# Optimization experiments

Measured on AMD Instinct MI355X. Metric: run time of the kernel, lower is better.

The kernel has to match this reference:

```python
import jax, jax.numpy as jnp
import numpy as np

B, C, N = 128, 256, 4096
CQ = C // 4
BN_EPS = 1e-5


def setup_inputs() -> dict:
    key = jax.random.key(0)
    ks = jax.random.split(key, 12)
    w = lambda k, shape: jax.random.normal(k, shape, dtype=jnp.float32) * 0.05
    return {
        "x": jax.random.normal(ks[0], (B, C, N), dtype=jnp.float32),
        "x_key": jax.random.normal(ks[1], (B, C, 1), dtype=jnp.float32),
        "wq": w(ks[2], (CQ, C)), "bq": jnp.zeros((CQ,), jnp.float32),
        "wk": w(ks[3], (CQ, C)), "bk": jnp.zeros((CQ,), jnp.float32),
        "wv": w(ks[4], (C, C)),  "bv": jnp.zeros((C,), jnp.float32),
        "wt": w(ks[5], (C, C)),  "bt": jnp.zeros((C,), jnp.float32),
        "gamma": jnp.ones((C,), jnp.float32),
        "beta": jnp.zeros((C,), jnp.float32),
    }


def reference(x, x_key, wq, bq, wk, bk, wv, bv, wt, bt, gamma, beta):
    # 1x1 convs are per-point linear maps over the channel dim.
    x_q = jnp.einsum('oc,bcn->bno', wq, x) + bq              # (B, N, C/4)
    x_k = jnp.einsum('oc,bcn->bo', wk, x_key) + bk           # (B, C/4)  (length-1 key)
    x_v = jnp.einsum('oc,bcn->bon', wv, x) + bv[None, :, None]  # (B, C, N)

    # tanh-gated QK: energy over the N points against the single key.
    energy = jnp.einsum('bno,bo->bn', jnp.tanh(x_q), jnp.tanh(x_k))  # (B, N)
    attention = jax.nn.softmax(energy, axis=-1)                       # (B, N)

    # context: attention-weighted sum of V -> single point per batch.
    x_r = jnp.einsum('bcn,bn->bc', x_v, attention)[..., None]  # (B, C, 1)

    # trans_conv + BatchNorm1d (training-mode batch stats) + ReLU + residual.
    t = jnp.einsum('oc,bcn->bon', wt, x_key - x_r) + bt[None, :, None]  # (B, C, 1)
    mean = t.mean(axis=(0, 2), keepdims=True)
    var = t.var(axis=(0, 2), keepdims=True)  # biased, as torch BN training
    t = (t - mean) * jax.lax.rsqrt(var + BN_EPS) * gamma[None, :, None] + beta[None, :, None]
    x_final = (x_key + jax.nn.relu(t))[..., 0]  # (B, C)
    return x_final, attention
```

## Files before the change

kernel.cpp:

```cpp
#include <hip/hip_runtime.h>
#include <math.h>

typedef _Float16 h4_t __attribute__((ext_vector_type(4)));
typedef _Float16 h8_t __attribute__((ext_vector_type(8)));
typedef float    f4_t __attribute__((ext_vector_type(4)));

#define NB 128
#define NC 256
#define NQ 64
#define NN 4096
#define TN 64
#define TPB 8
#define NGRP (NN / TN / TPB)

#define BAR_LGKM() do {                                              \
    asm volatile("s_waitcnt lgkmcnt(0)" ::: "memory");               \
    __builtin_amdgcn_s_barrier();                                    \
    asm volatile("" ::: "memory");                                   \
} while (0)

__device__ __forceinline__ float fast_tanh(float x) {
    float e = __builtin_amdgcn_exp2f(x * 2.885390082f);
    return 1.f - 2.f * __builtin_amdgcn_rcpf(e + 1.f);
}

__global__ void kpre(const float* __restrict__ wk, const float* __restrict__ bk,
                     const float* __restrict__ xkey, const float* __restrict__ wq,
                     float* __restrict__ kt, float* __restrict__ Mb,
                     _Float16* __restrict__ wqf)
{
    const int bid = blockIdx.x;
    const int tid = threadIdx.x;
    if (bid < 32) {
        const int b = bid * 4 + (tid >> 6);
        const int o = tid & 63;
        float a = bk[o];
        #pragma unroll 8
        for (int c = 0; c < NC; ++c)
            a += wk[o * NC + c] * xkey[b * NC + c];
        float t = tanhf(a);
        kt[b * NQ + o] = t;
        float m = fabsf(t);
        #pragma unroll
        for (int mm = 1; mm < 64; mm <<= 1) m += __shfl_xor(m, mm);
        if (o == 0) Mb[b] = m;
    } else {
        const int i = (bid - 32) * 256 + tid;
        const int j = i & 3;
        const int l = (i >> 2) & 63;
        const int f = i >> 8;
        const int ks = f >> 2, t = f & 3;
        const int o = t * 16 + (l & 15);
        const int c = ks * 16 + (l >> 4) * 4 + j;
        wqf[i] = (_Float16)wq[o * NC + c];
    }
}

template<int ATOMIC>
__global__ __launch_bounds__(256, 2) void k_main(
    const float* __restrict__ x, const _Float16* __restrict__ wqf,
    const float* __restrict__ bq, const float* __restrict__ kt,
    const float* __restrict__ Mb, float* __restrict__ w_out,
    float* __restrict__ spart, float* __restrict__ zpart,
    float* __restrict__ sraw, float* __restrict__ Zg)
{
    __shared__ _Float16 xl[64 * 256];
    __shared__ _Float16 wqf_l[16384];
    __shared__ float wsl[4][16];
    __shared__ float sacc[4][256];
    __shared__ float zsl[4];

    const int bid  = blockIdx.x;
    const int b    = bid >> 3;
    const int grp  = bid & 7;
    const int tid  = threadIdx.x;
    const int n    = tid & 63;
    const int cg   = tid >> 6;

    const int wid  = tid >> 6;
    const int lane = tid & 63;
    const int g    = lane >> 4;
    const int li   = lane & 15;

    const float* srcbase = x + ((size_t)b * NC + cg * 64) * NN + n;

    #pragma unroll
    for (int i = 0; i < 8; ++i)
        ((h8_t*)wqf_l)[i * 256 + tid] = ((const h8_t*)wqf)[i * 256 + tid];

    float ktv[4], bqv[4];
    #pragma unroll
    for (int q = 0; q < 4; ++q) {
        ktv[q] = kt[b * NQ + q * 16 + li];
        bqv[q] = bq[q * 16 + li];
    }
    const float Mbb = Mb[b];

    int n0 = grp * (TPB * TN);

    #define LOADC(dst, ch, off)                                                \
        { const float* _s = srcbase + (off);                                   \
          _Pragma("unroll")                                                    \
          for (int i = 0; i < 16; ++i)                                         \
              dst[i] = __builtin_nontemporal_load(&_s[(size_t)((ch)*16 + i) * NN]); }
    #define WRITEC(srcv, ch)                                                   \
        { _Pragma("unroll")                                                    \
          for (int k8 = 0; k8 < 2; ++k8) {                                     \
              h8_t h;                                                          \
              _Pragma("unroll")                                                \
              for (int j = 0; j < 8; ++j) h[j] = (_Float16)srcv[k8 * 8 + j];   \
              const int c   = cg * 64 + (ch) * 16 + k8 * 8;                    \
              const int idx = (n * 256 + c) ^ ((n & 7) << 3);                  \
              *(h8_t*)&xl[idx] = h;                                            \
          } }

    {
        float p0[16], p1[16], p2[16], p3[16];
        LOADC(p0, 0, n0); LOADC(p1, 1, n0); LOADC(p2, 2, n0); LOADC(p3, 3, n0);
        WRITEC(p0, 0); WRITEC(p1, 1); WRITEC(p2, 2); WRITEC(p3, 3);
    }
    BAR_LGKM();

    f4_t a2 = f4_t{0.f, 0.f, 0.f, 0.f};
    float zacc = 0.f;

    for (int t = 0; t < TPB; ++t) {
        const bool pf = (t + 1 < TPB);
        float c0[16], c1[16], c2[16], c3[16];
        if (pf) LOADC(c0, 0, n0 + TN);

        f4_t acc[4];
        #pragma unroll
        for (int q = 0; q < 4; ++q) acc[q] = f4_t{0.f, 0.f, 0.f, 0.f};
        #pragma unroll
        for (int ks = 0; ks < 8; ++ks) {
            const int nn   = wid * 16 + li;
            const int cA   = ks * 16 + g * 4;
            const int idxA = (nn * 256 + cA) ^ ((nn & 7) << 3);
            h4_t a = *(const h4_t*)&xl[idxA];
            #pragma unroll
            for (int q = 0; q < 4; ++q) {
                h4_t bf = *(const h4_t*)&wqf_l[((ks * 4 + q) * 64 + lane) * 4];
                acc[q] = __builtin_amdgcn_mfma_f32_16x16x16f16(a, bf, acc[q], 0, 0, 0);
            }
        }
        if (pf) LOADC(c1, 1, n0 + TN);
        #pragma unroll
        for (int ks = 8; ks < 16; ++ks) {
            const int nn   = wid * 16 + li;
            const int cA   = ks * 16 + g * 4;
            const int idxA = (nn * 256 + cA) ^ ((nn & 7) << 3);
            h4_t a = *(const h4_t*)&xl[idxA];
            #pragma unroll
            for (int q = 0; q < 4; ++q) {
                h4_t bf = *(const h4_t*)&wqf_l[((ks * 4 + q) * 64 + lane) * 4];
                acc[q] = __builtin_amdgcn_mfma_f32_16x16x16f16(a, bf, acc[q], 0, 0, 0);
            }
        }
        if (pf) LOADC(c2, 2, n0 + TN);

        float ep[4] = {0.f, 0.f, 0.f, 0.f};
        #pragma unroll
        for (int q = 0; q < 4; ++q) {
            #pragma unroll
            for (int r = 0; r < 4; ++r)
                ep[r] += fast_tanh(acc[q][r] + bqv[q]) * ktv[q];
        }
        #pragma unroll
        for (int r = 0; r < 4; ++r) {
            #pragma unroll
            for (int m = 1; m < 16; m <<= 1)
                ep[r] += __shfl_xor(ep[r], m);
        }
        if (pf) LOADC(c3, 3, n0 + TN);

        {
            f4_t wv;
            #pragma unroll
            for (int r = 0; r < 4; ++r)
                wv[r] = __builtin_amdgcn_exp2f((ep[r] - Mbb) * 1.44269504f);
            if (li == 0) {
                *(f4_t*)&w_out[b * NN + n0 + wid * 16 + g * 4] = wv;
                *(f4_t*)&wsl[wid][g * 4] = wv;
                zacc += wv[0] + wv[1] + wv[2] + wv[3];
            }
        }
        f4_t wrow[4];
        #pragma unroll
        for (int jj = 0; jj < 4; ++jj)
            wrow[jj] = *(const f4_t*)&wsl[wid][jj * 4];

        #pragma unroll
        for (int j = 0; j < 16; ++j) {
            const int nn  = wid * 16 + j;
            const int idx = (nn * 256 + 4 * lane) ^ ((nn & 7) << 3);
            h4_t xv = *(const h4_t*)&xl[idx];
            const float wj = wrow[j >> 2][j & 3];
            a2[0] += (float)xv[0] * wj;
            a2[1] += (float)xv[1] * wj;
            a2[2] += (float)xv[2] * wj;
            a2[3] += (float)xv[3] * wj;
        }

        BAR_LGKM();
        if (pf) { WRITEC(c0, 0); WRITEC(c1, 1); WRITEC(c2, 2); WRITEC(c3, 3); }
        n0 += TN;
        BAR_LGKM();
    }
    #undef LOADC
    #undef WRITEC

    {
        float z = zacc;
        z += __shfl_xor(z, 16);
        z += __shfl_xor(z, 32);
        if (lane == 0) zsl[wid] = z;
    }
    *(f4_t*)&sacc[wid][4 * lane] = a2;
    __syncthreads();

    const float ssum = sacc[0][tid] + sacc[1][tid] + sacc[2][tid] + sacc[3][tid];
    if (ATOMIC) {
        atomicAdd(&sraw[b * NC + tid], ssum);
        if (tid == 0) atomicAdd(&Zg[b], zsl[0] + zsl[1] + zsl[2] + zsl[3]);
    } else {
        spart[((size_t)(b * NGRP + grp)) * NC + tid] = ssum;
        if (tid == 0) zpart[b * NGRP + grp] = zsl[0] + zsl[1] + zsl[2] + zsl[3];
    }
}

__global__ void k2(const float* __restrict__ spart, const float* __restrict__ zpart,
                   const float* __restrict__ sraw,  const float* __restrict__ Zg,
                   const float* __restrict__ wv,    const float* __restrict__ wt,
                   const float* __restrict__ bv,    const float* __restrict__ bt,
                   const float* __restrict__ xkey,  float* __restrict__ tpre,
                   float* __restrict__ Zout, int atomicMode)
{
    const int b = blockIdx.x;
    const int tid = threadIdx.x;
    __shared__ float s_l[NC];
    __shared__ float d_l[NC];
    __shared__ float zsh;

    float ssum;
    if (atomicMode) {
        ssum = sraw[b * NC + tid];
        if (tid == 0) { zsh = Zg[b]; Zout[b] = zsh; }
    } else {
        ssum = 0.f;
        #pragma unroll
        for (int T = 0; T < NGRP; ++T)
            ssum += spart[((size_t)(b * NGRP + T)) * NC + tid];
        if (tid < NGRP) {
            float z = zpart[b * NGRP + tid];
            #pragma unroll
            for (int m = 1; m < NGRP; m <<= 1) z += __shfl_xor(z, m);
            if (tid == 0) { zsh = z; Zout[b] = z; }
        }
    }
    s_l[tid] = ssum;
    __syncthreads();

    const float invZ = 1.0f / zsh;
    {
        const f4_t* wrow = (const f4_t*)&wv[(size_t)tid * NC];
        float a = 0.f;
        #pragma unroll 8
        for (int k = 0; k < NC / 4; ++k) {
            const f4_t w4 = wrow[k];
            const f4_t s4 = *(const f4_t*)&s_l[k * 4];
            a += w4[0] * s4[0] + w4[1] * s4[1] + w4[2] * s4[2] + w4[3] * s4[3];
        }
        d_l[tid] = xkey[b * NC + tid] - (bv[tid] + a * invZ);
    }
    __syncthreads();
    {
        const f4_t* wrow = (const f4_t*)&wt[(size_t)tid * NC];
        float t = bt[tid];
        #pragma unroll 8
        for (int k = 0; k < NC / 4; ++k) {
            const f4_t w4 = wrow[k];
            const f4_t d4 = *(const f4_t*)&d_l[k * 4];
            t += w4[0] * d4[0] + w4[1] * d4[1] + w4[2] * d4[2] + w4[3] * d4[3];
        }
        tpre[b * NC + tid] = t;
    }
}

__global__ void kpost(const float* __restrict__ w, const float* __restrict__ Z,
                      const float* __restrict__ tpre, const float* __restrict__ xkey,
                      const float* __restrict__ gma, const float* __restrict__ bta,
                      float* __restrict__ attn_out, float* __restrict__ out)
{
    const int bid = blockIdx.x;
    if (bid < 2048) {
        const int i = bid * 256 + threadIdx.x;
        const int b = i >> 12;
        attn_out[i] = w[i] / Z[b];
        return;
    }
    __shared__ float sA[8][32], sB[8][32];
    __shared__ float mean_s[32], rs_s[32];
    const int cl = threadIdx.x & 31;
    const int bg = threadIdx.x >> 5;
    const int c  = (bid - 2048) * 32 + cl;

    float v[16];
    float s = 0.f, s2 = 0.f;
    #pragma unroll
    for (int i = 0; i < 16; ++i) {
        v[i] = tpre[(bg * 16 + i) * NC + c];
        s += v[i]; s2 += v[i] * v[i];
    }
    sA[bg][cl] = s; sB[bg][cl] = s2;
    __syncthreads();
    if (bg == 0) {
        float S = 0.f, S2 = 0.f;
        #pragma unroll
        for (int g2 = 0; g2 < 8; ++g2) { S += sA[g2][cl]; S2 += sB[g2][cl]; }
        const float mean = S * (1.f / NB);
        const float var  = S2 * (1.f / NB) - mean * mean;
        mean_s[cl] = mean;
        rs_s[cl]   = rsqrtf(var + 1e-5f);
    }
    __syncthreads();
    const float mean = mean_s[cl], rs = rs_s[cl];
    const float gc = gma[c], bc = bta[c];
    #pragma unroll
    for (int i = 0; i < 16; ++i) {
        float t2 = (v[i] - mean) * rs * gc + bc;
        t2 = t2 > 0.f ? t2 : 0.f;
        out[(bg * 16 + i) * NC + c] = xkey[(bg * 16 + i) * NC + c] + t2;
    }
}

extern "C" void kernel_launch(void* const* d_in, const int* in_sizes, int n_in,
                              void* d_out, int out_size, void* d_ws, size_t ws_size,
                              hipStream_t stream)
{
    const float* x    = (const float*)d_in[0];
    const float* xkey = (const float*)d_in[1];
    const float* wq   = (const float*)d_in[2];
    const float* bq   = (const float*)d_in[3];
    const float* wk   = (const float*)d_in[4];
    const float* bk   = (const float*)d_in[5];
    const float* wvm  = (const float*)d_in[6];
    const float* bv   = (const float*)d_in[7];
    const float* wtm  = (const float*)d_in[8];
    const float* bt   = (const float*)d_in[9];
    const float* gma  = (const float*)d_in[10];
    const float* bta  = (const float*)d_in[11];
    float* out = (float*)d_out;

    char* ws = (char*)d_ws;
    size_t off = 0;
    auto take = [&](size_t bytes) -> char* {
        char* p = ws + off;
        off = (off + bytes + 255) & ~(size_t)255;
        return p;
    };
    _Float16* wqf = (_Float16*)take(16384 * 2);
    float* kt   = (float*)take(NB * NQ * 4);
    float* Mb   = (float*)take(NB * 4);
    float* wbuf = (float*)take((size_t)NB * NN * 4);
    float* tpre = (float*)take(NB * NC * 4);
    float* Zf   = (float*)take(NB * 4);

    const size_t base = off;
    float* spart = (float*)take((size_t)NB * NGRP * NC * 4);
    float* zpart = (float*)take(NB * NGRP * 4);
    const bool det = (off <= ws_size);
    float* sraw = nullptr;
    float* Zg   = nullptr;
    if (!det) {
        off = base;
        sraw = (float*)take(NB * NC * 4);
        Zg   = (float*)take(NB * 4);
        hipMemsetAsync(sraw, 0, NB * NC * 4, stream);
        hipMemsetAsync(Zg, 0, NB * 4, stream);
    }

    kpre<<<96, 256, 0, stream>>>(wk, bk, xkey, wq, kt, Mb, wqf);
    if (det)
        k_main<0><<<NB * NGRP, 256, 0, stream>>>(x, wqf, bq, kt, Mb, wbuf,
                                                 spart, zpart, nullptr, nullptr);
    else
        k_main<1><<<NB * NGRP, 256, 0, stream>>>(x, wqf, bq, kt, Mb, wbuf,
                                                 nullptr, nullptr, sraw, Zg);
    k2<<<NB, 256, 0, stream>>>(spart, zpart, sraw, Zg, wvm, wtm, bv, bt, xkey,
                               tpre, Zf, det ? 0 : 1);
    kpost<<<2056, 256, 0, stream>>>(wbuf, Zf, tpre, xkey, gma, bta,
                                    out + NB * NC, out);
}
```

Measured before the change: 126.0 us.

## Use 512-thread blocks processing two 64-point tiles per iteration

The main kernel goes from 256 to 512 threads per block. Two waves groups each take one of two 64-point tiles per iteration from a doubled LDS buffer, and the grid halves to 4 groups per batch. The prefetch now issues all 64 loads at once at the top of the loop, instead of interleaving them through the MFMA phases. This aims to raise the bytes in flight per block and amortise barriers and the weight staging. In exchange LDS use doubles to about 100KB per block and register pressure rises, which may limit occupancy.

```diff
diff --git a/kernel.cpp b/kernel.cpp
--- a/kernel.cpp
+++ b/kernel.cpp
@@ -10,8 +10,8 @@
 #define NQ 64
 #define NN 4096
 #define TN 64
-#define TPB 8
-#define NGRP (NN / TN / TPB)
+#define PPB 8
+#define NGRP (NN / (2 * TN) / PPB)
 
 #define BAR_LGKM() do {                                              \
     asm volatile("s_waitcnt lgkmcnt(0)" ::: "memory");               \
@@ -57,36 +57,38 @@
 }
 
 template<int ATOMIC>
-__global__ __launch_bounds__(256, 2) void k_main(
+__global__ __launch_bounds__(512, 2) void k_main(
     const float* __restrict__ x, const _Float16* __restrict__ wqf,
     const float* __restrict__ bq, const float* __restrict__ kt,
     const float* __restrict__ Mb, float* __restrict__ w_out,
     float* __restrict__ spart, float* __restrict__ zpart,
     float* __restrict__ sraw, float* __restrict__ Zg)
 {
-    __shared__ _Float16 xl[64 * 256];
+    __shared__ _Float16 xl[2][64 * 256];
     __shared__ _Float16 wqf_l[16384];
-    __shared__ float wsl[4][16];
-    __shared__ float sacc[4][256];
-    __shared__ float zsl[4];
+    __shared__ float wsl[8][16];
+    __shared__ float sacc[8][256];
+    __shared__ float zsl[8];
 
     const int bid  = blockIdx.x;
-    const int b    = bid >> 3;
-    const int grp  = bid & 7;
+    const int b    = bid >> 2;
+    const int grp  = bid & 3;
     const int tid  = threadIdx.x;
     const int n    = tid & 63;
     const int cg   = tid >> 6;
 
-    const int wid  = tid >> 6;
+    const int w    = tid >> 6;
     const int lane = tid & 63;
     const int g    = lane >> 4;
     const int li   = lane & 15;
-
-    const float* srcbase = x + ((size_t)b * NC + cg * 64) * NN + n;
+    const int T    = w >> 2;
+    const int s    = w & 3;
+
+    const float* srcbase = x + ((size_t)b * NC + cg * 32) * NN + n;
 
     #pragma unroll
-    for (int i = 0; i < 8; ++i)
-        ((h8_t*)wqf_l)[i * 256 + tid] = ((const h8_t*)wqf)[i * 256 + tid];
+    for (int i = 0; i < 4; ++i)
+        ((h8_t*)wqf_l)[i * 512 + tid] = ((const h8_t*)wqf)[i * 512 + tid];
 
     float ktv[4], bqv[4];
     #pragma unroll
@@ -96,68 +98,58 @@
     }
     const float Mbb = Mb[b];
 
-    int n0 = grp * (TPB * TN);
-
-    #define LOADC(dst, ch, off)                                                \
-        { const float* _s = srcbase + (off);                                   \
-          _Pragma("unroll")                                                    \
-          for (int i = 0; i < 16; ++i)                                         \
-              dst[i] = __builtin_nontemporal_load(&_s[(size_t)((ch)*16 + i) * NN]); }
-    #define WRITEC(srcv, ch)                                                   \
+    int n0 = grp * (PPB * 2 * TN);
+
+    #define LOADP(dA, dB, off)                                                 \
         { _Pragma("unroll")                                                    \
-          for (int k8 = 0; k8 < 2; ++k8) {                                     \
+          for (int i = 0; i < 32; ++i) {                                       \
+              const float* _r = srcbase + (size_t)i * NN + (off);              \
+              dA[i] = __builtin_nontemporal_load(_r);                          \
+              dB[i] = __builtin_nontemporal_load(_r + TN);                     \
+          } }
+    #define WRITEP(srcv, buf)                                                  \
+        { _Pragma("unroll")                                                    \
+          for (int k8 = 0; k8 < 4; ++k8) {                                     \
               h8_t h;                                                          \
               _Pragma("unroll")                                                \
               for (int j = 0; j < 8; ++j) h[j] = (_Float16)srcv[k8 * 8 + j];   \
-              const int c   = cg * 64 + (ch) * 16 + k8 * 8;                    \
+              const int c   = cg * 32 + k8 * 8;                                \
               const int idx = (n * 256 + c) ^ ((n & 7) << 3);                  \
-              *(h8_t*)&xl[idx] = h;                                            \
+              *(h8_t*)&xl[buf][idx] = h;                                       \
           } }
 
     {
-        float p0[16], p1[16], p2[16], p3[16];
-        LOADC(p0, 0, n0); LOADC(p1, 1, n0); LOADC(p2, 2, n0); LOADC(p3, 3, n0);
-        WRITEC(p0, 0); WRITEC(p1, 1); WRITEC(p2, 2); WRITEC(p3, 3);
+        float pA[32], pB[32];
+        LOADP(pA, pB, n0);
+        WRITEP(pA, 0); WRITEP(pB, 1);
     }
     BAR_LGKM();
 
     f4_t a2 = f4_t{0.f, 0.f, 0.f, 0.f};
     float zacc = 0.f;
 
-    for (int t = 0; t < TPB; ++t) {
-        const bool pf = (t + 1 < TPB);
-        float c0[16], c1[16], c2[16], c3[16];
-        if (pf) LOADC(c0, 0, n0 + TN);
+    for (int p = 0; p < PPB; ++p) {
+        const bool pf = (p + 1 < PPB);
+        float cA[32], cB[32];
+        if (pf) LOADP(cA, cB, n0 + 2 * TN);
+
+        const int tn0 = n0 + T * TN;
 
         f4_t acc[4];
         #pragma unroll
         for (int q = 0; q < 4; ++q) acc[q] = f4_t{0.f, 0.f, 0.f, 0.f};
         #pragma unroll
-        for (int ks = 0; ks < 8; ++ks) {
-            const int nn   = wid * 16 + li;
-            const int cA   = ks * 16 + g * 4;
-            const int idxA = (nn * 256 + cA) ^ ((nn & 7) << 3);
-            h4_t a = *(const h4_t*)&xl[idxA];
+        for (int ks = 0; ks < 16; ++ks) {
+            const int nn   = s * 16 + li;
+            const int cA2  = ks * 16 + g * 4;
+            const int idxA = (nn * 256 + cA2) ^ ((nn & 7) << 3);
+            h4_t a = *(const h4_t*)&xl[T][idxA];
             #pragma unroll
             for (int q = 0; q < 4; ++q) {
                 h4_t bf = *(const h4_t*)&wqf_l[((ks * 4 + q) * 64 + lane) * 4];
                 acc[q] = __builtin_amdgcn_mfma_f32_16x16x16f16(a, bf, acc[q], 0, 0, 0);
             }
         }
-        if (pf) LOADC(c1, 1, n0 + TN);
-        #pragma unroll
-        for (int ks = 8; ks < 16; ++ks) {
-            const int nn   = wid * 16 + li;
-            const int cA   = ks * 16 + g * 4;
-            const int idxA = (nn * 256 + cA) ^ ((nn & 7) << 3);
-            h4_t a = *(const h4_t*)&xl[idxA];
-            #pragma unroll
-            for (int q = 0; q < 4; ++q) {
-                h4_t bf = *(const h4_t*)&wqf_l[((ks * 4 + q) * 64 + lane) * 4];
-                acc[q] = __builtin_amdgcn_mfma_f32_16x16x16f16(a, bf, acc[q], 0, 0, 0);
-            }
-        }
-        if (pf) LOADC(c2, 2, n0 + TN);
 
         float ep[4] = {0.f, 0.f, 0.f, 0.f};
         #pragma unroll
@@ -172,7 +164,6 @@
             for (int m = 1; m < 16; m <<= 1)
                 ep[r] += __shfl_xor(ep[r], m);
         }
-        if (pf) LOADC(c3, 3, n0 + TN);
 
         {
             f4_t wv;
@@ -180,21 +171,21 @@
             for (int r = 0; r < 4; ++r)
                 wv[r] = __builtin_amdgcn_exp2f((ep[r] - Mbb) * 1.44269504f);
             if (li == 0) {
-                *(f4_t*)&w_out[b * NN + n0 + wid * 16 + g * 4] = wv;
-                *(f4_t*)&wsl[wid][g * 4] = wv;
+                *(f4_t*)&w_out[b * NN + tn0 + s * 16 + g * 4] = wv;
+                *(f4_t*)&wsl[w][g * 4] = wv;
                 zacc += wv[0] + wv[1] + wv[2] + wv[3];
             }
         }
         f4_t wrow[4];
         #pragma unroll
         for (int jj = 0; jj < 4; ++jj)
-            wrow[jj] = *(const f4_t*)&wsl[wid][jj * 4];
+            wrow[jj] = *(const f4_t*)&wsl[w][jj * 4];
 
         #pragma unroll
         for (int j = 0; j < 16; ++j) {
-            const int nn  = wid * 16 + j;
+            const int nn  = s * 16 + j;
             const int idx = (nn * 256 + 4 * lane) ^ ((nn & 7) << 3);
-            h4_t xv = *(const h4_t*)&xl[idx];
+            h4_t xv = *(const h4_t*)&xl[T][idx];
             const float wj = wrow[j >> 2][j & 3];
             a2[0] += (float)xv[0] * wj;
             a2[1] += (float)xv[1] * wj;
@@ -203,29 +194,43 @@
         }
 
         BAR_LGKM();
-        if (pf) { WRITEC(c0, 0); WRITEC(c1, 1); WRITEC(c2, 2); WRITEC(c3, 3); }
-        n0 += TN;
+        if (pf) { WRITEP(cA, 0); WRITEP(cB, 1); }
+        n0 += 2 * TN;
         BAR_LGKM();
     }
-    #undef LOADC
-    #undef WRITEC
+    #undef LOADP
+    #undef WRITEP
 
     {
         float z = zacc;
         z += __shfl_xor(z, 16);
         z += __shfl_xor(z, 32);
-        if (lane == 0) zsl[wid] = z;
-    }
-    *(f4_t*)&sacc[wid][4 * lane] = a2;
-    __syncthreads();
-
-    const float ssum = sacc[0][tid] + sacc[1][tid] + sacc[2][tid] + sacc[3][tid];
-    if (ATOMIC) {
-        atomicAdd(&sraw[b * NC + tid], ssum);
-        if (tid == 0) atomicAdd(&Zg[b], zsl[0] + zsl[1] + zsl[2] + zsl[3]);
-    } else {
-        spart[((size_t)(b * NGRP + grp)) * NC + tid] = ssum;
-        if (tid == 0) zpart[b * NGRP + grp] = zsl[0] + zsl[1] + zsl[2] + zsl[3];
+        if (lane == 0) zsl[w] = z;
+    }
+    *(f4_t*)&sacc[w][4 * lane] = a2;
+    __syncthreads();
+
+    if (tid < NC) {
+        float ssum = 0.f;
+        #pragma unroll
+        for (int ww = 0; ww < 8; ++ww) ssum += sacc[ww][tid];
+        if (ATOMIC) {
+            atomicAdd(&sraw[b * NC + tid], ssum);
+            if (tid == 0) {
+                float zt = 0.f;
+                #pragma unroll
+                for (int ww = 0; ww < 8; ++ww) zt += zsl[ww];
+                atomicAdd(&Zg[b], zt);
+            }
+        } else {
+            spart[((size_t)(b * NGRP + grp)) * NC + tid] = ssum;
+            if (tid == 0) {
+                float zt = 0.f;
+                #pragma unroll
+                for (int ww = 0; ww < 8; ++ww) zt += zsl[ww];
+                zpart[b * NGRP + grp] = zt;
+            }
+        }
     }
 }
 
@@ -251,11 +256,11 @@
         #pragma unroll
         for (int T = 0; T < NGRP; ++T)
             ssum += spart[((size_t)(b * NGRP + T)) * NC + tid];
-        if (tid < NGRP) {
-            float z = zpart[b * NGRP + tid];
-            #pragma unroll
-            for (int m = 1; m < NGRP; m <<= 1) z += __shfl_xor(z, m);
-            if (tid == 0) { zsh = z; Zout[b] = z; }
+        if (tid == 0) {
+            float z = 0.f;
+            #pragma unroll
+            for (int T = 0; T < NGRP; ++T) z += zpart[b * NGRP + T];
+            zsh = z; Zout[b] = z;
         }
     }
     s_l[tid] = ssum;
@@ -382,10 +387,10 @@
 
     kpre<<<96, 256, 0, stream>>>(wk, bk, xkey, wq, kt, Mb, wqf);
     if (det)
-        k_main<0><<<NB * NGRP, 256, 0, stream>>>(x, wqf, bq, kt, Mb, wbuf,
+        k_main<0><<<NB * NGRP, 512, 0, stream>>>(x, wqf, bq, kt, Mb, wbuf,
                                                  spart, zpart, nullptr, nullptr);
     else
-        k_main<1><<<NB * NGRP, 256, 0, stream>>>(x, wqf, bq, kt, Mb, wbuf,
+        k_main<1><<<NB * NGRP, 512, 0, stream>>>(x, wqf, bq, kt, Mb, wbuf,
                                                  nullptr, nullptr, sraw, Zg);
     k2<<<NB, 256, 0, stream>>>(spart, zpart, sraw, Zg, wvm, wtm, bv, bt, xkey,
                                tpre, Zf, det ? 0 : 1);
```

After: 138.4 us. 9.9% more time.
